# Kernel tuning notes

Measured on AMD Instinct MI355X. Metric: run time of the kernel, lower is better.

## Reference

```python
import jax, jax.numpy as jnp
import numpy as np

M = 4096   # nodes per layer (also number of input nodes)
L = 32     # internal layers
K = 64     # in-degree of each internal node


def setup_inputs() -> dict:
    key = jax.random.key(0)
    k_x, k_wi, k_bi, k_w, k_b, k_g = jax.random.split(key, 6)
    x = jax.random.normal(k_x, (M, 1), dtype=jnp.float32)
    w_in = jax.random.normal(k_wi, (M, 1), dtype=jnp.float32)
    b_in = jax.random.normal(k_bi, (M,), dtype=jnp.float32)
    # scale internal weights so sigmoid(K-term dot) is not fully saturated
    w = jax.random.normal(k_w, (L, M, K), dtype=jnp.float32) * 0.05
    b = jax.random.normal(k_b, (L, M), dtype=jnp.float32)
    # predecessor indices into the previous layer's value vector
    igraf = jax.random.randint(k_g, (L, M, K), 0, M, dtype=jnp.int32)
    return {"x": x, "w_in": w_in, "b_in": b_in, "w": w, "b": b, "igraf": igraf}


def reference(x, w_in, b_in, w, b, igraf):
    # input nodes: relu(Linear(1,1)) applied to each scalar input, vectorized
    v = jax.nn.relu(w_in[:, 0] * x[:, 0] + b_in)          # [M]
    # internal nodes, layer by layer (topological order):
    # each node gathers K predecessor values and applies sigmoid(Linear(K,1))
    for l in range(L):
        g = v[igraf[l]]                                   # [M, K] irregular gather
        v = jax.nn.sigmoid(jnp.einsum('mk,mk->m', w[l], g) + b[l])
    # original returns values[n_nodes - 1] (shape [1])
    return v[-1:]
```

## Files before the change

### kernel.cpp

```cpp
#include <hip/hip_runtime.h>

#define M 4096
#define L 32
#define K 64
#define NBLK 64
#define BLOCK 256
#define NPB 64
#define EPT 16
#define FB 0xAAAAAAAAu

__global__ __launch_bounds__(BLOCK)
void net_kernel(const float* __restrict__ x,
                const float* __restrict__ w_in,
                const float* __restrict__ b_in,
                const float* __restrict__ w,
                const float* __restrict__ b,
                const int* __restrict__ igraf,
                float* __restrict__ out,
                unsigned long long* __restrict__ buf)
{
    __shared__ float sv[M];

    const int tid   = threadIdx.x;
    const int blk   = blockIdx.x;
    const int node  = blk * NPB + (tid >> 2);
    const int chunk = tid & 3;
    const bool pub  = (chunk == 0);
    const bool lastblk = (blk == NBLK - 1);

    float4 wv[4]; int4 iv[4]; float breg = 0.0f;
    {
        const size_t f0 = (size_t)node * K + (size_t)chunk * EPT;
        const float4* wp = (const float4*)(w + f0);
        const int4*   ip = (const int4*)(igraf + f0);
        wv[0] = wp[0]; wv[1] = wp[1]; wv[2] = wp[2]; wv[3] = wp[3];
        iv[0] = ip[0]; iv[1] = ip[1]; iv[2] = ip[2]; iv[3] = ip[3];
        if (pub) breg = b[node];
    }

    #pragma unroll
    for (int j = 0; j < 4; ++j) {
        const int idx = tid + j * BLOCK;
        const float4 x4 = ((const float4*)x)[idx];
        const float4 wi = ((const float4*)w_in)[idx];
        const float4 bi = ((const float4*)b_in)[idx];
        float4 r;
        r.x = fmaxf(fmaf(wi.x, x4.x, bi.x), 0.0f);
        r.y = fmaxf(fmaf(wi.y, x4.y, bi.y), 0.0f);
        r.z = fmaxf(fmaf(wi.z, x4.z, bi.z), 0.0f);
        r.w = fmaxf(fmaf(wi.w, x4.w, bi.w), 0.0f);
        ((float4*)sv)[idx] = r;
    }
    __syncthreads();

    for (int t = 0; t < L; ++t) {
        float p = 0.0f;
        #pragma unroll
        for (int q = 0; q < 4; ++q) {
            p = fmaf(wv[q].x, sv[iv[q].x], p);
            p = fmaf(wv[q].y, sv[iv[q].y], p);
            p = fmaf(wv[q].z, sv[iv[q].z], p);
            p = fmaf(wv[q].w, sv[iv[q].w], p);
        }
        p += __shfl_xor(p, 1, 64);
        p += __shfl_xor(p, 2, 64);

        float val = 0.0f;
        if (pub) val = 1.0f / (1.0f + __expf(-(p + breg)));

        if (t == L - 1) {
            if (tid == 252) out[0] = val;
            break;
        }

        if (pub) {
            const unsigned long long pk =
                ((unsigned long long)(FB + (unsigned)(t + 1)) << 32) |
                (unsigned long long)__float_as_uint(val);
            __hip_atomic_store(&buf[(size_t)t * M + node], pk,
                               __ATOMIC_RELAXED, __HIP_MEMORY_SCOPE_AGENT);
        }

        if (t == L - 2 && !lastblk) return;

        {
            const size_t nb = ((size_t)(t + 1) * M + (size_t)node) * K
                            + (size_t)chunk * EPT;
            const float4* wp = (const float4*)(w + nb);
            const int4*   ip = (const int4*)(igraf + nb);
            wv[0] = wp[0]; wv[1] = wp[1]; wv[2] = wp[2]; wv[3] = wp[3];
            iv[0] = ip[0]; iv[1] = ip[1]; iv[2] = ip[2]; iv[3] = ip[3];
            if (pub) breg = b[(t + 1) * M + node];
        }

        const unsigned long long* src = buf + (size_t)t * M;
        unsigned long long vals[16];
        #pragma unroll
        for (int j = 0; j < 16; ++j)
            vals[j] = __hip_atomic_load(&src[tid + j * BLOCK],
                                        __ATOMIC_RELAXED,
                                        __HIP_MEMORY_SCOPE_AGENT);

        __syncthreads();

        const unsigned tag = FB + (unsigned)(t + 1);
        for (;;) {
            bool ok = true;
            #pragma unroll
            for (int j = 0; j < 16; ++j) {
                if ((unsigned)(vals[j] >> 32) != tag) {
                    ok = false;
                    vals[j] = __hip_atomic_load(&src[tid + j * BLOCK],
                                                __ATOMIC_RELAXED,
                                                __HIP_MEMORY_SCOPE_AGENT);
                }
            }
            if (ok) break;
        }

        #pragma unroll
        for (int j = 0; j < 16; ++j)
            sv[tid + j * BLOCK] = __uint_as_float((unsigned)vals[j]);
        __syncthreads();
    }
}

extern "C" void kernel_launch(void* const* d_in, const int* in_sizes, int n_in,
                              void* d_out, int out_size, void* d_ws, size_t ws_size,
                              hipStream_t stream) {
    const float* x     = (const float*)d_in[0];
    const float* w_in  = (const float*)d_in[1];
    const float* b_in  = (const float*)d_in[2];
    const float* wt    = (const float*)d_in[3];
    const float* b     = (const float*)d_in[4];
    const int*   igraf = (const int*)d_in[5];
    float*       out   = (float*)d_out;

    unsigned long long* buf = (unsigned long long*)d_ws;

    hipLaunchKernelGGL(net_kernel, dim3(NBLK), dim3(BLOCK), 0, stream,
                       x, w_in, b_in, wt, b, igraf, out, buf);
    (void)in_sizes; (void)n_in; (void)out_size; (void)ws_size;
}
```

Before: 160.3 us.

## Double-buffer shared values, widen block to 512 threads, and drop a barrier per layer

Doubles the block to 512 threads with 8 threads per node, so each thread gathers 8 predecessors and polls 8 buffer entries instead of 16. Adds a second shared value buffer so the pre-poll __syncthreads can be removed. Staggers each block's polling start by block index to spread contention. Issues the polling loads before the next layer's weight loads. The cost is more threads per block, a third shuffle stage, and twice the shared memory.

```diff
diff --git a/kernel.cpp b/kernel.cpp
--- a/kernel.cpp
+++ b/kernel.cpp
@@ -4,9 +4,12 @@
 #define L 32
 #define K 64
 #define NBLK 64
-#define BLOCK 256
+#define BLOCK 512
 #define NPB 64
-#define EPT 16
+#define TPN 8
+#define EPT 8
+#define ENT 8
+#define MK (M * K)
 #define FB 0xAAAAAAAAu
 
 __global__ __launch_bounds__(BLOCK)
@@ -19,27 +22,27 @@
                 float* __restrict__ out,
                 unsigned long long* __restrict__ buf)
 {
-    __shared__ float sv[M];
+    __shared__ float sv[2][M];
 
     const int tid   = threadIdx.x;
     const int blk   = blockIdx.x;
-    const int node  = blk * NPB + (tid >> 2);
-    const int chunk = tid & 3;
+    const int node  = blk * NPB + (tid >> 3);
+    const int chunk = tid & 7;
     const bool pub  = (chunk == 0);
     const bool lastblk = (blk == NBLK - 1);
 
-    float4 wv[4]; int4 iv[4]; float breg = 0.0f;
+    float4 wv0, wv1; int4 iv0, iv1; float breg;
     {
         const size_t f0 = (size_t)node * K + (size_t)chunk * EPT;
         const float4* wp = (const float4*)(w + f0);
         const int4*   ip = (const int4*)(igraf + f0);
-        wv[0] = wp[0]; wv[1] = wp[1]; wv[2] = wp[2]; wv[3] = wp[3];
-        iv[0] = ip[0]; iv[1] = ip[1]; iv[2] = ip[2]; iv[3] = ip[3];
-        if (pub) breg = b[node];
+        wv0 = wp[0]; wv1 = wp[1];
+        iv0 = ip[0]; iv1 = ip[1];
+        breg = b[node];
     }
 
     #pragma unroll
-    for (int j = 0; j < 4; ++j) {
+    for (int j = 0; j < 2; ++j) {
         const int idx = tid + j * BLOCK;
         const float4 x4 = ((const float4*)x)[idx];
         const float4 wi = ((const float4*)w_in)[idx];
@@ -49,27 +52,29 @@
         r.y = fmaxf(fmaf(wi.y, x4.y, bi.y), 0.0f);
         r.z = fmaxf(fmaf(wi.z, x4.z, bi.z), 0.0f);
         r.w = fmaxf(fmaf(wi.w, x4.w, bi.w), 0.0f);
-        ((float4*)sv)[idx] = r;
+        ((float4*)sv[0])[idx] = r;
     }
     __syncthreads();
 
     for (int t = 0; t < L; ++t) {
-        float p = 0.0f;
-        #pragma unroll
-        for (int q = 0; q < 4; ++q) {
-            p = fmaf(wv[q].x, sv[iv[q].x], p);
-            p = fmaf(wv[q].y, sv[iv[q].y], p);
-            p = fmaf(wv[q].z, sv[iv[q].z], p);
-            p = fmaf(wv[q].w, sv[iv[q].w], p);
-        }
+        const float* svc = sv[t & 1];
+        float p;
+        p = wv0.x * svc[iv0.x];
+        p = fmaf(wv0.y, svc[iv0.y], p);
+        p = fmaf(wv0.z, svc[iv0.z], p);
+        p = fmaf(wv0.w, svc[iv0.w], p);
+        p = fmaf(wv1.x, svc[iv1.x], p);
+        p = fmaf(wv1.y, svc[iv1.y], p);
+        p = fmaf(wv1.z, svc[iv1.z], p);
+        p = fmaf(wv1.w, svc[iv1.w], p);
         p += __shfl_xor(p, 1, 64);
         p += __shfl_xor(p, 2, 64);
+        p += __shfl_xor(p, 4, 64);
 
-        float val = 0.0f;
-        if (pub) val = 1.0f / (1.0f + __expf(-(p + breg)));
+        const float val = 1.0f / (1.0f + __expf(-(p + breg)));
 
         if (t == L - 1) {
-            if (tid == 252) out[0] = val;
+            if (tid == 504) out[0] = val;
             break;
         }
 
@@ -83,34 +88,34 @@
 
         if (t == L - 2 && !lastblk) return;
 
+        const unsigned long long* src = buf + (size_t)t * M;
+        unsigned long long vals[ENT]; int eidx[ENT];
+        #pragma unroll
+        for (int j = 0; j < ENT; ++j) {
+            eidx[j] = (tid + j * BLOCK + blk * NPB) & (M - 1);
+            vals[j] = __hip_atomic_load(&src[eidx[j]],
+                                        __ATOMIC_RELAXED,
+                                        __HIP_MEMORY_SCOPE_AGENT);
+        }
+
         {
-            const size_t nb = ((size_t)(t + 1) * M + (size_t)node) * K
+            const size_t nb = (size_t)(t + 1) * MK + (size_t)node * K
                             + (size_t)chunk * EPT;
             const float4* wp = (const float4*)(w + nb);
             const int4*   ip = (const int4*)(igraf + nb);
-            wv[0] = wp[0]; wv[1] = wp[1]; wv[2] = wp[2]; wv[3] = wp[3];
-            iv[0] = ip[0]; iv[1] = ip[1]; iv[2] = ip[2]; iv[3] = ip[3];
-            if (pub) breg = b[(t + 1) * M + node];
+            wv0 = wp[0]; wv1 = wp[1];
+            iv0 = ip[0]; iv1 = ip[1];
+            breg = b[(t + 1) * M + node];
         }
-
-        const unsigned long long* src = buf + (size_t)t * M;
-        unsigned long long vals[16];
-        #pragma unroll
-        for (int j = 0; j < 16; ++j)
-            vals[j] = __hip_atomic_load(&src[tid + j * BLOCK],
-                                        __ATOMIC_RELAXED,
-                                        __HIP_MEMORY_SCOPE_AGENT);
-
-        __syncthreads();
 
         const unsigned tag = FB + (unsigned)(t + 1);
         for (;;) {
             bool ok = true;
             #pragma unroll
-            for (int j = 0; j < 16; ++j) {
+            for (int j = 0; j < ENT; ++j) {
                 if ((unsigned)(vals[j] >> 32) != tag) {
                     ok = false;
-                    vals[j] = __hip_atomic_load(&src[tid + j * BLOCK],
+                    vals[j] = __hip_atomic_load(&src[eidx[j]],
                                                 __ATOMIC_RELAXED,
                                                 __HIP_MEMORY_SCOPE_AGENT);
                 }
@@ -118,9 +123,10 @@
             if (ok) break;
         }
 
+        float* svn = sv[(t + 1) & 1];
         #pragma unroll
-        for (int j = 0; j < 16; ++j)
-            sv[tid + j * BLOCK] = __uint_as_float((unsigned)vals[j]);
+        for (int j = 0; j < ENT; ++j)
+            svn[eidx[j]] = __uint_as_float((unsigned)vals[j]);
         __syncthreads();
     }
 }
```

New measurement: 180.6 us. 12.6% more time.
